# Kernel tuning notes

Hardware: AMD Instinct MI355X
Metric: run time of the kernel (lower is better)

Reference implementation:

```python
import jax, jax.numpy as jnp
import numpy as np
import math


def setup_inputs() -> dict:
    key = jax.random.key(0)
    k1, k2, k3 = jax.random.split(key, 3)
    img = jax.random.normal(k1, (32, 3, 512, 512), dtype=jnp.float32)
    c_u = jax.random.normal(k2, (100, 100), dtype=jnp.float32)  # scalar-field mode coeffs for dx
    c_v = jax.random.normal(k3, (100, 100), dtype=jnp.float32)  # scalar-field mode coeffs for dy
    return {"img": img, "c_u": c_u, "c_v": c_v}


def _scalar_field(c, n):
    # random scalar field of size n x n from the first m modes (m = c.shape[0])
    m = c.shape[0]
    x = jnp.linspace(0.0, 1.0, n, dtype=c.dtype)            # [n]
    k = jnp.arange(1, m + 1, dtype=c.dtype)                 # [m]
    i, j = jnp.meshgrid(k, k, indexing='ij')                # [m, m]
    r = jnp.sqrt(i ** 2 + j ** 2)
    e = (r < m + 0.5).astype(c.dtype) / r                   # sqrt(1/energy) per mode
    s = jnp.sin(jnp.pi * x[:, None] * k[None, :])           # [n, m]
    return jnp.einsum('ij,xi,yj->yx', c * e, s, s)          # [n, n]


def reference(img, c_u, c_v):
    n = img.shape[-1]  # square image assumed (n x n)
    m = c_u.shape[0]   # frequency cutoff `cut`

    # temperature_range(n, cut), deterministic T = midpoint of allowed range (alpha=1)
    log_cut = math.log(m + 1e-06)
    T1 = 1.0 / (math.pi * n ** 2 * log_cut)
    T2 = 4.0 / (math.pi ** 3 * m ** 2 * log_cut)
    T2 = max(T1, T2)
    T = 0.5 * (T1 + T2)

    # displacement fields [n, n]
    dx = (T ** 0.5) * _scalar_field(c_u, n) * n
    dy = (T ** 0.5) * _scalar_field(c_v, n) * n

    # remap with bilinear ('linear') interpolation
    dtype = dx.dtype
    y, x = jnp.meshgrid(jnp.arange(n, dtype=dtype), jnp.arange(n, dtype=dtype), indexing='ij')
    xn = jnp.clip(x - dx, 0.0, n - 1)
    yn = jnp.clip(y - dy, 0.0, n - 1)

    xf = jnp.floor(xn).astype(jnp.int32)
    yf = jnp.floor(yn).astype(jnp.int32)
    xc = jnp.ceil(xn).astype(jnp.int32)
    yc = jnp.ceil(yn).astype(jnp.int32)
    xv = xn - xf.astype(dtype)
    yv = yn - yf.astype(dtype)

    out = ((1 - yv) * (1 - xv) * img[..., yf, xf]
           + (1 - yv) * xv * img[..., yf, xc]
           + yv * (1 - xv) * img[..., yc, xf]
           + yv * xv * img[..., yc, xc])
    return out
```

## Files before the change

### kernel.cpp

```cpp
#include <hip/hip_runtime.h>
#include <math.h>

#define NN 512
#define MM 100
#define TPB 256
#define ROWS_OUT 4
#define ROWS_LDS 13
#define PXPT 8

typedef float f32x4 __attribute__((ext_vector_type(4)));
typedef unsigned int u32;
typedef u32 u32x2 __attribute__((ext_vector_type(2)));


__global__ void sin_table_kernel(float* __restrict__ St) {
    int tid = blockIdx.x * blockDim.x + threadIdx.x;
    if (tid >= NN * MM) return;
    int x = tid / MM, j = tid % MM;
    double arg = M_PI * ((double)x / (double)(NN - 1)) * (double)(j + 1);
    St[tid] = (float)sin(arg);
}

__global__ void bcoef_kernel(const float* __restrict__ St,
                             const float* __restrict__ c_u,
                             const float* __restrict__ c_v,
                             float* __restrict__ B_u,
                             float* __restrict__ B_v) {
    int x = blockIdx.x;
    int j = threadIdx.x;
    if (j >= MM) return;
    float au = 0.f, av = 0.f;
    for (int i = 0; i < MM; ++i) {
        int i1 = i + 1, j1 = j + 1;
        int r2i = i1 * i1 + j1 * j1;
        float w = (r2i <= 10100) ? (1.0f / sqrtf((float)r2i)) : 0.0f;
        float sw = St[x * MM + i] * w;
        au += sw * c_u[i * MM + j];
        av += sw * c_v[i * MM + j];
    }
    B_u[j * NN + x] = au;
    B_v[j * NN + x] = av;
}

__global__ __launch_bounds__(256)
void field_weights_kernel(const float* __restrict__ St,
                          const float* __restrict__ B_u,
                          const float* __restrict__ B_v,
                          float scale,
                          u32x2* __restrict__ pk,
                          int* __restrict__ strip_tab) {
    __shared__ float sS[ROWS_OUT * MM];
    __shared__ int s_mn[4], s_mx[4];
    int t = threadIdx.x;
    int strip = blockIdx.x;
    int y0 = strip * ROWS_OUT;

    for (int i = t; i < ROWS_OUT * MM; i += 256) {
        int r = i / MM, j = i % MM;
        sS[i] = St[(y0 + r) * MM + j];
    }
    __syncthreads();

    float au[ROWS_OUT][2] = {}, av[ROWS_OUT][2] = {};
    for (int j = 0; j < MM; ++j) {
        float bu0 = B_u[j * NN + t], bu1 = B_u[j * NN + t + 256];
        float bv0 = B_v[j * NN + t], bv1 = B_v[j * NN + t + 256];
        #pragma unroll
        for (int r = 0; r < ROWS_OUT; ++r) {
            float s = sS[r * MM + j];
            au[r][0] += bu0 * s; au[r][1] += bu1 * s;
            av[r][0] += bv0 * s; av[r][1] += bv1 * s;
        }
    }

    float xvq[PXPT], yvq[PXPT];
    int offA[PXPT], offB[PXPT];
    int myf = NN, Myc = -1;
    #pragma unroll
    for (int i = 0; i < PXPT; ++i) {
        int c = i & 1, r = i >> 1;
        int xi = (c << 8) + t;
        int yi = y0 + r;
        float xn = fminf(fmaxf((float)xi - scale * au[r][c], 0.0f), (float)(NN - 1));
        float yn = fminf(fmaxf((float)yi - scale * av[r][c], 0.0f), (float)(NN - 1));
        int xf = (int)floorf(xn), yf = (int)floorf(yn);
        int yc = (int)ceilf(yn);
        xvq[i] = xn - (float)xf;
        yvq[i] = yn - (float)yf;
        offA[i] = (yf << 9) + xf;
        offB[i] = (yc << 9) + xf;
        myf = min(myf, yf);
        Myc = max(Myc, yc);
    }

    for (int d = 32; d; d >>= 1) {
        myf = min(myf, __shfl_xor(myf, d));
        Myc = max(Myc, __shfl_xor(Myc, d));
    }
    int wid = t >> 6;
    if ((t & 63) == 0) { s_mn[wid] = myf; s_mx[wid] = Myc; }
    __syncthreads();
    int r0 = min(min(s_mn[0], s_mn[1]), min(s_mn[2], s_mn[3]));
    int nr = max(max(s_mx[0], s_mx[1]), max(s_mx[2], s_mx[3])) - r0 + 1;
    if (t == 0) { strip_tab[2 * strip] = r0; strip_tab[2 * strip + 1] = nr; }

    int rb = r0 << 9;
    #pragma unroll
    for (int i = 0; i < PXPT; ++i) {
        int pix = ((y0 + (i >> 1)) << 9) + ((i & 1) << 8) + t;
        u32 oa = (u32)(offA[i] - rb);
        u32 ob = (u32)(offB[i] - rb);
        u32 xq = (u32)__float2int_rn(xvq[i] * 65535.0f);
        u32 yq = (u32)__float2int_rn(yvq[i] * 65535.0f);
        u32x2 v; v[0] = oa | (ob << 16); v[1] = xq | (yq << 16);
        pk[pix] = v;
    }
}

__global__ __launch_bounds__(TPB, 6)
void remap_kernel(const float* __restrict__ img,
                  const u32x2* __restrict__ pk,
                  const int* __restrict__ strip_tab,
                  float* __restrict__ out,
                  int planes) {
    __shared__ __align__(16) float rows[ROWS_LDS * NN + 1];

    int nb = gridDim.x;
    int bid = blockIdx.x;
    int sid = (bid & 7) * (nb >> 3) + (bid >> 3);
    int plane = sid >> 7;
    int strip = sid & 127;

    int t = threadIdx.x;
    int r0 = strip_tab[2 * strip];
    int nr = strip_tab[2 * strip + 1];

    const float* __restrict__ ip = img + (size_t)plane * (NN * NN);
    float* __restrict__ op = out + (size_t)plane * (NN * NN);
    int base = ((strip * ROWS_OUT) << 9) + t;

    const float qs = 1.0f / 65535.0f;

    if (nr <= ROWS_LDS) {
        if (t == 0) rows[nr * NN] = 0.f;

        int nbytes = nr << 11;
        int wave = t >> 6;
        int lane_goff = t * 16;
        const char* ipc = (const char*)(ip + (r0 << 9));
        for (int ob = 0; ob < nbytes; ob += TPB * 16) {
            if (ob + wave * 1024 < nbytes) {
                __builtin_amdgcn_global_load_lds(
                    (const __attribute__((address_space(1))) void*)(ipc + ob + lane_goff),
                    (__attribute__((address_space(3))) void*)((char*)rows + ob + wave * 1024),
                    16, 0, 0);
            }
        }
        __syncthreads();

        #pragma unroll
        for (int i = 0; i < PXPT; ++i) {
            int pix = base + ((i >> 1) << 9) + ((i & 1) << 8);
            u32x2 p = pk[pix];
            int oA = (int)(p[0] & 0xFFFFu);
            int oB = (int)(p[0] >> 16);
            float xv = (float)(p[1] & 0xFFFFu) * qs;
            float yv = (float)(p[1] >> 16) * qs;
            float omx = 1.f - xv, omy = 1.f - yv;
            float top = omx * rows[oA] + xv * rows[oA + 1];
            float bot = omx * rows[oB] + xv * rows[oB + 1];
            float o = omy * top + yv * bot;
            __builtin_nontemporal_store(o, op + pix);
        }
    } else {
        int rb = r0 << 9;
        #pragma unroll
        for (int i = 0; i < PXPT; ++i) {
            int pix = base + ((i >> 1) << 9) + ((i & 1) << 8);
            u32x2 p = pk[pix];
            int a = (int)(p[0] & 0xFFFFu) + rb;
            int b = (int)(p[0] >> 16) + rb;
            float xv = (float)(p[1] & 0xFFFFu) * qs;
            float yv = (float)(p[1] >> 16) * qs;
            float omx = 1.f - xv, omy = 1.f - yv;
            int e1 = ((a & 511) == 511) ? 0 : 1;
            float top = omx * ip[a] + xv * ip[a + e1];
            float bot = omx * ip[b] + xv * ip[b + e1];
            float o = omy * top + yv * bot;
            __builtin_nontemporal_store(o, op + pix);
        }
    }
}

extern "C" void kernel_launch(void* const* d_in, const int* in_sizes, int n_in,
                              void* d_out, int out_size, void* d_ws, size_t ws_size,
                              hipStream_t stream) {
    const float* img = (const float*)d_in[0];
    const float* c_u = (const float*)d_in[1];
    const float* c_v = (const float*)d_in[2];
    float* out = (float*)d_out;

    int planes = in_sizes[0] / (NN * NN);

    float* ws   = (float*)d_ws;
    float* St   = ws;
    float* B_u  = St + NN * MM;
    float* B_v  = B_u + MM * NN;
    u32x2* pk   = (u32x2*)(ws + 153600);
    int* strip_tab = (int*)(ws + 153600 + 2 * NN * NN);

    double log_cut = log((double)MM + 1e-6);
    double T1 = 1.0 / (M_PI * (double)NN * (double)NN * log_cut);
    double T2 = 4.0 / (M_PI * M_PI * M_PI * (double)MM * (double)MM * log_cut);
    if (T2 < T1) T2 = T1;
    double T = 0.5 * (T1 + T2);
    float scale = (float)(sqrt(T) * (double)NN);

    sin_table_kernel<<<(NN * MM + 255) / 256, 256, 0, stream>>>(St);
    bcoef_kernel<<<NN, 128, 0, stream>>>(St, c_u, c_v, B_u, B_v);
    field_weights_kernel<<<NN / ROWS_OUT, 256, 0, stream>>>(St, B_u, B_v, scale,
                                                            pk, strip_tab);

    int strips = NN / ROWS_OUT;
    remap_kernel<<<strips * planes, TPB, 0, stream>>>(img, pk, strip_tab,
                                                      out, planes);
}
```

Baseline: 80.95 us.

## Fuse sine table into coefficient kernels and vectorize remap to two pixels per thread

Removes the separate sine-table kernel by computing sine values inside the bcoef and field-weights kernels, dropping one launch and a global table round trip. The remap kernel now processes two adjacent pixels per thread per row, using 16-byte loads of packed weights and 8-byte nontemporal stores. This cuts memory instruction count but changes the LDS access pattern and recomputes some sines redundantly in double precision.

```diff
diff --git a/kernel.cpp b/kernel.cpp
--- a/kernel.cpp
+++ b/kernel.cpp
@@ -8,33 +8,31 @@
 #define ROWS_LDS 13
 #define PXPT 8
 
-typedef float f32x4 __attribute__((ext_vector_type(4)));
+typedef float f32x2 __attribute__((ext_vector_type(2)));
 typedef unsigned int u32;
 typedef u32 u32x2 __attribute__((ext_vector_type(2)));
-
-
-__global__ void sin_table_kernel(float* __restrict__ St) {
-    int tid = blockIdx.x * blockDim.x + threadIdx.x;
-    if (tid >= NN * MM) return;
-    int x = tid / MM, j = tid % MM;
-    double arg = M_PI * ((double)x / (double)(NN - 1)) * (double)(j + 1);
-    St[tid] = (float)sin(arg);
-}
-
-__global__ void bcoef_kernel(const float* __restrict__ St,
-                             const float* __restrict__ c_u,
+typedef u32 u32x4 __attribute__((ext_vector_type(4)));
+
+
+__global__ void bcoef_kernel(const float* __restrict__ c_u,
                              const float* __restrict__ c_v,
                              float* __restrict__ B_u,
                              float* __restrict__ B_v) {
+    __shared__ float sSt[MM];
     int x = blockIdx.x;
     int j = threadIdx.x;
+    if (j < MM) {
+        double arg = M_PI * ((double)x / (double)(NN - 1)) * (double)(j + 1);
+        sSt[j] = (float)sin(arg);
+    }
+    __syncthreads();
     if (j >= MM) return;
     float au = 0.f, av = 0.f;
     for (int i = 0; i < MM; ++i) {
         int i1 = i + 1, j1 = j + 1;
         int r2i = i1 * i1 + j1 * j1;
         float w = (r2i <= 10100) ? (1.0f / sqrtf((float)r2i)) : 0.0f;
-        float sw = St[x * MM + i] * w;
+        float sw = sSt[i] * w;
         au += sw * c_u[i * MM + j];
         av += sw * c_v[i * MM + j];
     }
@@ -43,8 +41,7 @@
 }
 
 __global__ __launch_bounds__(256)
-void field_weights_kernel(const float* __restrict__ St,
-                          const float* __restrict__ B_u,
+void field_weights_kernel(const float* __restrict__ B_u,
                           const float* __restrict__ B_v,
                           float scale,
                           u32x2* __restrict__ pk,
@@ -57,7 +54,8 @@
 
     for (int i = t; i < ROWS_OUT * MM; i += 256) {
         int r = i / MM, j = i % MM;
-        sS[i] = St[(y0 + r) * MM + j];
+        double arg = M_PI * ((double)(y0 + r) / (double)(NN - 1)) * (double)(j + 1);
+        sS[i] = (float)sin(arg);
     }
     __syncthreads();
 
@@ -137,9 +135,10 @@
 
     const float* __restrict__ ip = img + (size_t)plane * (NN * NN);
     float* __restrict__ op = out + (size_t)plane * (NN * NN);
-    int base = ((strip * ROWS_OUT) << 9) + t;
+    int base = ((strip * ROWS_OUT) << 9) + (t << 1);
 
     const float qs = 1.0f / 65535.0f;
+    const u32x4* __restrict__ pk4 = (const u32x4*)pk;
 
     if (nr <= ROWS_LDS) {
         if (t == 0) rows[nr * NN] = 0.f;
@@ -159,35 +158,46 @@
         __syncthreads();
 
         #pragma unroll
-        for (int i = 0; i < PXPT; ++i) {
-            int pix = base + ((i >> 1) << 9) + ((i & 1) << 8);
-            u32x2 p = pk[pix];
-            int oA = (int)(p[0] & 0xFFFFu);
-            int oB = (int)(p[0] >> 16);
-            float xv = (float)(p[1] & 0xFFFFu) * qs;
-            float yv = (float)(p[1] >> 16) * qs;
-            float omx = 1.f - xv, omy = 1.f - yv;
-            float top = omx * rows[oA] + xv * rows[oA + 1];
-            float bot = omx * rows[oB] + xv * rows[oB + 1];
-            float o = omy * top + yv * bot;
-            __builtin_nontemporal_store(o, op + pix);
+        for (int r = 0; r < ROWS_OUT; ++r) {
+            int pix = base + (r << 9);
+            u32x4 p = pk4[pix >> 1];
+            int oA0 = (int)(p[0] & 0xFFFFu), oB0 = (int)(p[0] >> 16);
+            float xv0 = (float)(p[1] & 0xFFFFu) * qs;
+            float yv0 = (float)(p[1] >> 16) * qs;
+            int oA1 = (int)(p[2] & 0xFFFFu), oB1 = (int)(p[2] >> 16);
+            float xv1 = (float)(p[3] & 0xFFFFu) * qs;
+            float yv1 = (float)(p[3] >> 16) * qs;
+            float t0 = (1.f - xv0) * rows[oA0] + xv0 * rows[oA0 + 1];
+            float b0 = (1.f - xv0) * rows[oB0] + xv0 * rows[oB0 + 1];
+            float t1 = (1.f - xv1) * rows[oA1] + xv1 * rows[oA1 + 1];
+            float b1 = (1.f - xv1) * rows[oB1] + xv1 * rows[oB1 + 1];
+            f32x2 o;
+            o[0] = (1.f - yv0) * t0 + yv0 * b0;
+            o[1] = (1.f - yv1) * t1 + yv1 * b1;
+            __builtin_nontemporal_store(o, (f32x2*)(op + pix));
         }
     } else {
         int rb = r0 << 9;
         #pragma unroll
-        for (int i = 0; i < PXPT; ++i) {
-            int pix = base + ((i >> 1) << 9) + ((i & 1) << 8);
-            u32x2 p = pk[pix];
-            int a = (int)(p[0] & 0xFFFFu) + rb;
-            int b = (int)(p[0] >> 16) + rb;
-            float xv = (float)(p[1] & 0xFFFFu) * qs;
-            float yv = (float)(p[1] >> 16) * qs;
-            float omx = 1.f - xv, omy = 1.f - yv;
-            int e1 = ((a & 511) == 511) ? 0 : 1;
-            float top = omx * ip[a] + xv * ip[a + e1];
-            float bot = omx * ip[b] + xv * ip[b + e1];
-            float o = omy * top + yv * bot;
-            __builtin_nontemporal_store(o, op + pix);
+        for (int r = 0; r < ROWS_OUT; ++r) {
+            int pix = base + (r << 9);
+            u32x4 p = pk4[pix >> 1];
+            int a0 = (int)(p[0] & 0xFFFFu) + rb, b0i = (int)(p[0] >> 16) + rb;
+            float xv0 = (float)(p[1] & 0xFFFFu) * qs;
+            float yv0 = (float)(p[1] >> 16) * qs;
+            int a1 = (int)(p[2] & 0xFFFFu) + rb, b1i = (int)(p[2] >> 16) + rb;
+            float xv1 = (float)(p[3] & 0xFFFFu) * qs;
+            float yv1 = (float)(p[3] >> 16) * qs;
+            int e0 = ((a0 & 511) == 511) ? 0 : 1;
+            int e1 = ((a1 & 511) == 511) ? 0 : 1;
+            float t0 = (1.f - xv0) * ip[a0] + xv0 * ip[a0 + e0];
+            float bo0 = (1.f - xv0) * ip[b0i] + xv0 * ip[b0i + e0];
+            float t1 = (1.f - xv1) * ip[a1] + xv1 * ip[a1 + e1];
+            float bo1 = (1.f - xv1) * ip[b1i] + xv1 * ip[b1i + e1];
+            f32x2 o;
+            o[0] = (1.f - yv0) * t0 + yv0 * bo0;
+            o[1] = (1.f - yv1) * t1 + yv1 * bo1;
+            __builtin_nontemporal_store(o, (f32x2*)(op + pix));
         }
     }
 }
@@ -203,11 +213,10 @@
     int planes = in_sizes[0] / (NN * NN);
 
     float* ws   = (float*)d_ws;
-    float* St   = ws;
-    float* B_u  = St + NN * MM;
+    float* B_u  = ws;
     float* B_v  = B_u + MM * NN;
-    u32x2* pk   = (u32x2*)(ws + 153600);
-    int* strip_tab = (int*)(ws + 153600 + 2 * NN * NN);
+    u32x2* pk   = (u32x2*)(ws + 2 * MM * NN);
+    int* strip_tab = (int*)(ws + 2 * MM * NN + 2 * NN * NN);
 
     double log_cut = log((double)MM + 1e-6);
     double T1 = 1.0 / (M_PI * (double)NN * (double)NN * log_cut);
@@ -216,9 +225,8 @@
     double T = 0.5 * (T1 + T2);
     float scale = (float)(sqrt(T) * (double)NN);
 
-    sin_table_kernel<<<(NN * MM + 255) / 256, 256, 0, stream>>>(St);
-    bcoef_kernel<<<NN, 128, 0, stream>>>(St, c_u, c_v, B_u, B_v);
-    field_weights_kernel<<<NN / ROWS_OUT, 256, 0, stream>>>(St, B_u, B_v, scale,
+    bcoef_kernel<<<NN, 128, 0, stream>>>(c_u, c_v, B_u, B_v);
+    field_weights_kernel<<<NN / ROWS_OUT, 256, 0, stream>>>(B_u, B_v, scale,
                                                             pk, strip_tab);
 
     int strips = NN / ROWS_OUT;
```

Result: faster. 75.87 us (-6.3%).
